# Kernel tuning notes

Hardware: AMD Instinct MI355X
Metric: run time of the kernel (lower is better)

Reference implementation:

```python
import jax, jax.numpy as jnp
import numpy as np

B, T, N, K, DEG = 4, 256, 4096, 64, 4
L = T - 1                # number of transition steps
NNZ = B * N * DEG        # COO entries per step


def setup_inputs() -> dict:
    key = jax.random.key(0)
    k1, k2, k3, k4, k5 = jax.random.split(key, 5)
    observation = jax.random.normal(k1, (B, T, K), dtype=jnp.float32)
    W_em = jax.random.normal(k2, (K, N), dtype=jnp.float32) * 0.05
    duration = jax.random.randint(k3, (B,), 1, T + 1)  # in [1, T]
    # COO layout: for each batch b and each source state s, DEG outgoing edges
    src = jnp.tile(jnp.repeat(jnp.arange(N, dtype=jnp.int32), DEG), (B,))   # [NNZ]
    bidx = jnp.repeat(jnp.arange(B, dtype=jnp.int32), N * DEG)              # [NNZ]
    tgt = jax.random.randint(k4, (L, NNZ), 0, N, dtype=jnp.int32)
    # guarantee a self-loop so every target state has >=1 incoming edge
    self_mask = (jnp.arange(NNZ) % DEG) == 0
    tgt = jnp.where(self_mask[None, :], src[None, :], tgt)
    trans_idx = jnp.stack([jnp.broadcast_to(bidx, (L, NNZ)),
                           jnp.broadcast_to(src, (L, NNZ)),
                           tgt], axis=-1)                                   # [L,NNZ,3]
    trans_logvals = jnp.log(jax.random.uniform(k5, (L, NNZ), minval=0.1, maxval=1.0,
                                               dtype=jnp.float32))
    return {"observation": observation, "W_em": W_em, "duration": duration,
            "trans_idx": trans_idx, "trans_logvals": trans_logvals}


def _forward_alpha(observation, W_em, trans_idx, trans_logvals):
    # emission log-probs [B,T,N]
    em = jax.nn.log_softmax(jnp.einsum('btk,kn->btn', observation, W_em), axis=-1)
    la0 = em[:, 0, :] - jnp.log(jnp.float32(N))  # uniform start distribution

    def step(la_prev, inp):
        idx, lv, e = inp  # idx [NNZ,3], lv [NNZ], e [B,N]
        b, s, t = idx[:, 0], idx[:, 1], idx[:, 2]
        seg = b * N + t
        contrib = la_prev[b, s] + lv  # log_alpha[b,src] + log A[b,src,tgt]
        # numerically-stable segmented logsumexp over incoming edges per (b,tgt)
        m = jax.ops.segment_max(contrib, seg, num_segments=B * N)
        m_safe = jnp.where(jnp.isfinite(m), m, 0.0)
        ssum = jax.ops.segment_sum(jnp.exp(contrib - m_safe[seg]), seg,
                                   num_segments=B * N)
        ssum_safe = jnp.where(ssum > 0, ssum, 1.0)
        la = jnp.where(ssum > 0, jnp.log(ssum_safe) + m_safe, -jnp.inf)
        la = la.reshape(B, N) + e
        return la, la

    em_t = jnp.swapaxes(em, 0, 1)  # [T,B,N]
    _, las = jax.lax.scan(step, la0, (trans_idx, trans_logvals, em_t[1:]))
    log_alpha = jnp.concatenate([la0[None], las], axis=0)  # [T,B,N]
    return jnp.swapaxes(log_alpha, 0, 1)  # [B,T,N]


def reference(observation, W_em, duration, trans_idx, trans_logvals):
    log_alpha = _forward_alpha(observation, W_em, trans_idx, trans_logvals)
    log_sums = jax.nn.logsumexp(log_alpha, axis=2)                # [B,T]
    log_probs = jnp.take_along_axis(log_sums, duration[:, None] - 1, axis=1)  # [B,1]
    return log_probs
```

## Files before the change

### kernel.cpp

```cpp
#include <hip/hip_runtime.h>
#include <hip/hip_bf16.h>

#define Bc 4
#define Tc 256
#define Nc 4096
#define Kc 64
#define DEGc 4
#define Lc (Tc - 1)
#define NNZc (Bc * Nc * DEGc)
#define NPB 8
#define TPB 512
#define TPB_EM 256
#define NODES_PER (Nc / NPB)
#define INV_N (1.0f / 4096.0f)

typedef float f32x4 __attribute__((ext_vector_type(4)));

__device__ __forceinline__ float cohLoadF(const float* p) {
  return __hip_atomic_load((float*)p, __ATOMIC_RELAXED, __HIP_MEMORY_SCOPE_AGENT);
}
__device__ __forceinline__ void cohStore4(float* p, f32x4 v) {
  asm volatile("global_store_dwordx4 %0, %1, off sc0 sc1" :: "v"(p), "v"(v) : "memory");
}

template <int NT>
__device__ __forceinline__ float blockSumT(float v, volatile float* red) {
#pragma unroll
  for (int o = 1; o < 64; o <<= 1) v += __shfl_xor(v, o, 64);
  __syncthreads();
  if ((threadIdx.x & 63) == 0) red[threadIdx.x >> 6] = v;
  __syncthreads();
  float s = 0.f;
#pragma unroll
  for (int k = 0; k < NT / 64; ++k) s += red[k];
  return s;
}
template <int NT>
__device__ __forceinline__ float blockMaxT(float v, volatile float* red) {
#pragma unroll
  for (int o = 1; o < 64; o <<= 1) v = fmaxf(v, __shfl_xor(v, o, 64));
  __syncthreads();
  if ((threadIdx.x & 63) == 0) red[threadIdx.x >> 6] = v;
  __syncthreads();
  float m = -INFINITY;
#pragma unroll
  for (int k = 0; k < NT / 64; ++k) m = fmaxf(m, red[k]);
  return m;
}

__global__ __launch_bounds__(TPB_EM) void em_kernel(const float* __restrict__ obs,
                                                    const float* __restrict__ W,
                                                    float* __restrict__ emexp) {
  const int r = blockIdx.x, tid = threadIdx.x;
  __shared__ float o[Kc];
  __shared__ float red[8];
  if (tid < Kc) o[tid] = obs[(size_t)r * Kc + tid];
  __syncthreads();
  float4 acc[4];
#pragma unroll
  for (int gI = 0; gI < 4; ++gI) acc[gI] = make_float4(0.f, 0.f, 0.f, 0.f);
  const float4* W4 = (const float4*)W;
  for (int k = 0; k < Kc; ++k) {
    const float ov = o[k];
    const float4* wr = W4 + (size_t)k * (Nc / 4);
#pragma unroll
    for (int gI = 0; gI < 4; ++gI) {
      float4 w = wr[gI * 256 + tid];
      acc[gI].x = fmaf(ov, w.x, acc[gI].x);
      acc[gI].y = fmaf(ov, w.y, acc[gI].y);
      acc[gI].z = fmaf(ov, w.z, acc[gI].z);
      acc[gI].w = fmaf(ov, w.w, acc[gI].w);
    }
  }
  float m = -INFINITY;
#pragma unroll
  for (int gI = 0; gI < 4; ++gI)
    m = fmaxf(m, fmaxf(fmaxf(acc[gI].x, acc[gI].y), fmaxf(acc[gI].z, acc[gI].w)));
  m = blockMaxT<TPB_EM>(m, red);
  float s = 0.f;
#pragma unroll
  for (int gI = 0; gI < 4; ++gI)
    s += __expf(acc[gI].x - m) + __expf(acc[gI].y - m) + __expf(acc[gI].z - m) + __expf(acc[gI].w - m);
  s = blockSumT<TPB_EM>(s, red);
  const float lse = m + __logf(s);
  float4* em4 = (float4*)emexp;
#pragma unroll
  for (int gI = 0; gI < 4; ++gI) {
    float4 w = acc[gI];
    w.x = __expf(w.x - lse); w.y = __expf(w.y - lse);
    w.z = __expf(w.z - lse); w.w = __expf(w.w - lse);
    em4[(size_t)r * (Nc / 4) + gI * 256 + tid] = w;
  }
}

__device__ __forceinline__ void publish(unsigned long long* slot, unsigned t, float sp) {
  union { float f; unsigned u; } c; c.f = sp;
  unsigned long long v = ((unsigned long long)c.u << 32) | (unsigned long long)t;
  __hip_atomic_store(slot, v, __ATOMIC_RELAXED, __HIP_MEMORY_SCOPE_AGENT);
}
__device__ __forceinline__ float pollFlags(unsigned long long* fb, int parity, unsigned t) {
  unsigned long long* base = fb + parity * 8;
  for (;;) {
    unsigned long long v[8];
#pragma unroll
    for (int k = 0; k < 8; ++k)
      v[k] = __hip_atomic_load(&base[k], __ATOMIC_RELAXED, __HIP_MEMORY_SCOPE_AGENT);
    bool ok = true;
    float s = 0.f;
#pragma unroll
    for (int k = 0; k < 8; ++k) {
      ok &= ((unsigned)(v[k] & 0xffffffffull) >= t);
      union { unsigned u; float f; } c; c.u = (unsigned)(v[k] >> 32);
      s += c.f;
    }
    if (ok) return s;
  }
}

__global__ __launch_bounds__(TPB) void scan_kernel(
    const int* __restrict__ duration,
    const int* __restrict__ tidx,
    const float* __restrict__ tlv,
    const float* __restrict__ emexp,
    float* __restrict__ part,
    unsigned long long* __restrict__ flags,
    float* __restrict__ out) {
  const int g = blockIdx.x;
  const int b = g / NPB, sl = g % NPB;
  const int tid = threadIdx.x;
  __shared__ float red[TPB / 64];
  __shared__ float lsb[Nc];
  __shared__ float sprev_sh;

  const int node = sl * NODES_PER + tid;
  const size_t ebase = (size_t)b * (Nc * DEGc) + (size_t)node * DEGc;
  unsigned long long* fb = flags + (size_t)b * 16;
  const int tstar = duration[b] - 1;

#pragma unroll
  for (int i = 0; i < Nc / TPB; ++i) lsb[i * TPB + tid] = 0.f;

  float v = emexp[((size_t)b * Tc) * Nc + node] * INV_N;
  float Spart = blockSumT<TPB>(v, red);
  float inv_sprev = 1.0f;
  float acc = 0.f;

  int4 c0, c1, c2; float4 cl; float em_cur;
  {
    const int4* ip = (const int4*)tidx + ((ebase * 3) >> 2);
    c0 = ip[0]; c1 = ip[1]; c2 = ip[2];
    cl = ((const float4*)tlv)[ebase >> 2];
    em_cur = emexp[((size_t)b * Tc + 1) * Nc + node];
  }

  for (int t = 1; t <= tstar; ++t) {
    const float a = v * inv_sprev;
    atomicAdd(&lsb[c0.z], a * __expf(cl.x));
    atomicAdd(&lsb[c1.y], a * __expf(cl.y));
    atomicAdd(&lsb[c2.x], a * __expf(cl.z));
    atomicAdd(&lsb[c2.w], a * __expf(cl.w));
    __syncthreads();

    float* pp = part + (((size_t)(t & 1) * Bc + b) * NPB + sl) * Nc;
    {
      f32x4 w0 = *(const f32x4*)&lsb[tid * 8];
      f32x4 w1 = *(const f32x4*)&lsb[tid * 8 + 4];
      *(f32x4*)&lsb[tid * 8] = (f32x4)0.0f;
      *(f32x4*)&lsb[tid * 8 + 4] = (f32x4)0.0f;
      cohStore4(&pp[tid * 8], w0);
      cohStore4(&pp[tid * 8 + 4], w1);
    }
    __syncthreads();

    if (tid == 0) {
      asm volatile("s_waitcnt vmcnt(0)" ::: "memory");
      publish(&fb[(t & 1) * 8 + sl], (unsigned)t, Spart);
    }

    int4 m0 = c0, m1 = c1, m2 = c2; float4 ml = cl; float em_nxt = em_cur;
    if (t < tstar) {
      const size_t e = (size_t)t * NNZc + ebase;
      const int4* ip = (const int4*)tidx + ((e * 3) >> 2);
      m0 = ip[0]; m1 = ip[1]; m2 = ip[2];
      ml = ((const float4*)tlv)[e >> 2];
      em_nxt = emexp[((size_t)b * Tc + t + 1) * Nc + node];
    }

    if (tid == 0) {
      float sp = pollFlags(fb, t & 1, (unsigned)t);
      sprev_sh = sp;
      if (sl == 0 && t <= tstar - 1) acc += __logf(sp);
    }
    __syncthreads();
    const float sprev = sprev_sh;

    const float* pbase = part + ((size_t)(t & 1) * Bc + b) * NPB * Nc;
    float pk[NPB];
#pragma unroll
    for (int k = 0; k < NPB; ++k) pk[k] = cohLoadF(&pbase[(size_t)k * Nc + node]);
    float sv = 0.f;
#pragma unroll
    for (int k = 0; k < NPB; ++k) sv += pk[k];
    v = sv * em_cur;
    Spart = blockSumT<TPB>(v, red);
    inv_sprev = __frcp_rn(sprev);

    c0 = m0; c1 = m1; c2 = m2; cl = ml; em_cur = em_nxt;
  }

  __syncthreads();
  if (tid == 0) {
    publish(&fb[((tstar + 1) & 1) * 8 + sl], (unsigned)(tstar + 1), Spart);
    if (sl == 0) {
      float sf = pollFlags(fb, (tstar + 1) & 1, (unsigned)(tstar + 1));
      out[b] = acc + __logf(sf);
    }
  }
}

extern "C" void kernel_launch(void* const* d_in, const int* in_sizes, int n_in,
                              void* d_out, int out_size, void* d_ws, size_t ws_size,
                              hipStream_t stream) {
  const float* obs = (const float*)d_in[0];
  const float* W = (const float*)d_in[1];
  const int* duration = (const int*)d_in[2];
  const int* tidx = (const int*)d_in[3];
  const float* tlv = (const float*)d_in[4];
  float* out = (float*)d_out;

  float* emexp = (float*)d_ws;
  float* part = emexp + (size_t)Bc * Tc * Nc;
  unsigned long long* flags = (unsigned long long*)(part + (size_t)2 * Bc * NPB * Nc);

  (void)hipMemsetAsync(flags, 0, Bc * 16 * sizeof(unsigned long long), stream);

  em_kernel<<<dim3(Bc * Tc), dim3(TPB_EM), 0, stream>>>(obs, W, emexp);
  scan_kernel<<<dim3(Bc * NPB), dim3(TPB), 0, stream>>>(duration, tidx, tlv, emexp,
                                                        part, flags, out);
}
```

Measured before the change: 1.775 ms.

## Pre-sort transitions by target into CSR and run single-block-per-batch pull scan

Adds a parallel sort kernel that buckets every step's COO edges by target state into a packed CSR (16-bit source plus fp16 edge weight) with row offsets. The sequential scan then runs as one 1024-thread block per batch that gathers incoming edges from shared memory. This replaces the shared-memory atomic scatter and the cross-block flag polling used before. The emission kernel now computes four timesteps per block and skips timesteps beyond each batch's duration. The trade-offs are fp16 rounding of transition probabilities and less parallelism in the serial scan, with only four blocks active.

```diff
diff --git a/kernel.cpp b/kernel.cpp
--- a/kernel.cpp
+++ b/kernel.cpp
@@ -1,27 +1,19 @@
 #include <hip/hip_runtime.h>
-#include <hip/hip_bf16.h>
+#include <hip/hip_fp16.h>
+
 
 #define Bc 4
 #define Tc 256
 #define Nc 4096
 #define Kc 64
-#define DEGc 4
 #define Lc (Tc - 1)
-#define NNZc (Bc * Nc * DEGc)
-#define NPB 8
-#define TPB 512
-#define TPB_EM 256
-#define NODES_PER (Nc / NPB)
+#define NNZb (Nc * 4)
+#define NNZc (Bc * NNZb)
+#define EROW 4104
 #define INV_N (1.0f / 4096.0f)
 
-typedef float f32x4 __attribute__((ext_vector_type(4)));
-
-__device__ __forceinline__ float cohLoadF(const float* p) {
-  return __hip_atomic_load((float*)p, __ATOMIC_RELAXED, __HIP_MEMORY_SCOPE_AGENT);
-}
-__device__ __forceinline__ void cohStore4(float* p, f32x4 v) {
-  asm volatile("global_store_dwordx4 %0, %1, off sc0 sc1" :: "v"(p), "v"(v) : "memory");
-}
+typedef unsigned int u32;
+typedef unsigned short u16;
 
 template <int NT>
 __device__ __forceinline__ float blockSumT(float v, volatile float* red) {
@@ -48,174 +40,233 @@
   return m;
 }
 
-__global__ __launch_bounds__(TPB_EM) void em_kernel(const float* __restrict__ obs,
-                                                    const float* __restrict__ W,
-                                                    float* __restrict__ emexp) {
-  const int r = blockIdx.x, tid = threadIdx.x;
-  __shared__ float o[Kc];
+__global__ __launch_bounds__(256) void em_kernel(const float* __restrict__ obs,
+                                                 const float* __restrict__ W,
+                                                 const int* __restrict__ duration,
+                                                 float* __restrict__ emexp) {
+  const int blk = blockIdx.x, tid = threadIdx.x;
+  const int b = blk >> 6;
+  const int t0 = (blk & 63) << 2;
+  if (t0 > duration[b] - 1) return;
+  const int rbase = b * Tc + t0;
+  __shared__ float osh[4][Kc];
   __shared__ float red[8];
-  if (tid < Kc) o[tid] = obs[(size_t)r * Kc + tid];
-  __syncthreads();
-  float4 acc[4];
-#pragma unroll
-  for (int gI = 0; gI < 4; ++gI) acc[gI] = make_float4(0.f, 0.f, 0.f, 0.f);
+  osh[tid >> 6][tid & 63] = obs[(size_t)(rbase + (tid >> 6)) * Kc + (tid & 63)];
+  __syncthreads();
+  float4 acc[4][4];
+#pragma unroll
+  for (int r = 0; r < 4; ++r)
+#pragma unroll
+    for (int g = 0; g < 4; ++g) acc[r][g] = make_float4(0.f, 0.f, 0.f, 0.f);
   const float4* W4 = (const float4*)W;
   for (int k = 0; k < Kc; ++k) {
-    const float ov = o[k];
-    const float4* wr = W4 + (size_t)k * (Nc / 4);
-#pragma unroll
-    for (int gI = 0; gI < 4; ++gI) {
-      float4 w = wr[gI * 256 + tid];
-      acc[gI].x = fmaf(ov, w.x, acc[gI].x);
-      acc[gI].y = fmaf(ov, w.y, acc[gI].y);
-      acc[gI].z = fmaf(ov, w.z, acc[gI].z);
-      acc[gI].w = fmaf(ov, w.w, acc[gI].w);
-    }
-  }
-  float m = -INFINITY;
-#pragma unroll
-  for (int gI = 0; gI < 4; ++gI)
-    m = fmaxf(m, fmaxf(fmaxf(acc[gI].x, acc[gI].y), fmaxf(acc[gI].z, acc[gI].w)));
-  m = blockMaxT<TPB_EM>(m, red);
+#pragma unroll
+    for (int g = 0; g < 4; ++g) {
+      const float4 w = W4[(size_t)k * (Nc / 4) + g * 256 + tid];
+#pragma unroll
+      for (int r = 0; r < 4; ++r) {
+        const float ov = osh[r][k];
+        acc[r][g].x = fmaf(ov, w.x, acc[r][g].x);
+        acc[r][g].y = fmaf(ov, w.y, acc[r][g].y);
+        acc[r][g].z = fmaf(ov, w.z, acc[r][g].z);
+        acc[r][g].w = fmaf(ov, w.w, acc[r][g].w);
+      }
+    }
+  }
+  float4* em4 = (float4*)emexp;
+#pragma unroll
+  for (int r = 0; r < 4; ++r) {
+    float m = -INFINITY;
+#pragma unroll
+    for (int g = 0; g < 4; ++g)
+      m = fmaxf(m, fmaxf(fmaxf(acc[r][g].x, acc[r][g].y), fmaxf(acc[r][g].z, acc[r][g].w)));
+    m = blockMaxT<256>(m, red);
+    float s = 0.f;
+#pragma unroll
+    for (int g = 0; g < 4; ++g)
+      s += __expf(acc[r][g].x - m) + __expf(acc[r][g].y - m) +
+           __expf(acc[r][g].z - m) + __expf(acc[r][g].w - m);
+    s = blockSumT<256>(s, red);
+    const float lse = m + __logf(s);
+#pragma unroll
+    for (int g = 0; g < 4; ++g) {
+      float4 w = acc[r][g];
+      w.x = __expf(w.x - lse); w.y = __expf(w.y - lse);
+      w.z = __expf(w.z - lse); w.w = __expf(w.w - lse);
+      em4[(size_t)(rbase + r) * (Nc / 4) + g * 256 + tid] = w;
+    }
+  }
+}
+
+__global__ __launch_bounds__(1024) void sort_kernel(const int* __restrict__ duration,
+                                                    const int* __restrict__ tidx,
+                                                    const float* __restrict__ tlv,
+                                                    u32* __restrict__ ce,
+                                                    u16* __restrict__ ends) {
+  const int rb = blockIdx.x;
+  const int b = rb & 3, row = rb >> 2;
+  if (row > duration[b] - 2) return;
+  const int tid = threadIdx.x;
+  __shared__ u32 cnt[Nc];
+  __shared__ u32 wred[16];
+  *(uint4*)&cnt[tid << 2] = make_uint4(0, 0, 0, 0);
+  __syncthreads();
+
+  const size_t ebase = (size_t)row * NNZc + (size_t)b * NNZb + (size_t)(tid << 4);
+  const int4* ip = (const int4*)tidx + ((ebase * 3) >> 2);
+  int4 c[12];
+#pragma unroll
+  for (int i = 0; i < 12; ++i) c[i] = ip[i];
+  const float4* lp = (const float4*)tlv + (ebase >> 2);
+  float4 lv[4];
+#pragma unroll
+  for (int g = 0; g < 4; ++g) lv[g] = lp[g];
+  u32 tg[16];
+#pragma unroll
+  for (int g = 0; g < 4; ++g) {
+    tg[4 * g + 0] = (u32)c[3 * g + 0].z;
+    tg[4 * g + 1] = (u32)c[3 * g + 1].y;
+    tg[4 * g + 2] = (u32)c[3 * g + 2].x;
+    tg[4 * g + 3] = (u32)c[3 * g + 2].w;
+  }
+#pragma unroll
+  for (int k = 0; k < 16; ++k) atomicAdd(&cnt[tg[k]], 1u);
+  __syncthreads();
+
+  uint4 c4 = *(uint4*)&cnt[tid << 2];
+  const u32 s = c4.x + c4.y + c4.z + c4.w;
+  u32 sc = s;
+#pragma unroll
+  for (int o = 1; o < 64; o <<= 1) {
+    u32 nv = __shfl_up(sc, o, 64);
+    if ((tid & 63) >= o) sc += nv;
+  }
+  if ((tid & 63) == 63) wred[tid >> 6] = sc;
+  __syncthreads();
+  if (tid < 64) {
+    u32 wv = (tid < 16) ? wred[tid] : 0;
+#pragma unroll
+    for (int o = 1; o < 16; o <<= 1) {
+      u32 nv = __shfl_up(wv, o, 64);
+      if (tid >= o) wv += nv;
+    }
+    if (tid < 16) wred[tid] = wv;
+  }
+  __syncthreads();
+  const u32 base = sc - s + ((tid >> 6) ? wred[(tid >> 6) - 1] : 0u);
+  cnt[(tid << 2) + 0] = base;
+  cnt[(tid << 2) + 1] = base + c4.x;
+  cnt[(tid << 2) + 2] = base + c4.x + c4.y;
+  cnt[(tid << 2) + 3] = base + c4.x + c4.y + c4.z;
+  __syncthreads();
+
+  u32* ceRow = ce + (size_t)rb * NNZb;
+#pragma unroll
+  for (int g = 0; g < 4; ++g) {
+    const u32 src = (u32)((tid << 2) + g);
+    const float l0 = lv[g].x, l1 = lv[g].y, l2 = lv[g].z, l3 = lv[g].w;
+    u32 pos;
+    pos = atomicAdd(&cnt[tg[4 * g + 0]], 1u);
+    ceRow[pos] = src | ((u32)__half_as_ushort(__float2half_rn(__expf(l0))) << 16);
+    pos = atomicAdd(&cnt[tg[4 * g + 1]], 1u);
+    ceRow[pos] = src | ((u32)__half_as_ushort(__float2half_rn(__expf(l1))) << 16);
+    pos = atomicAdd(&cnt[tg[4 * g + 2]], 1u);
+    ceRow[pos] = src | ((u32)__half_as_ushort(__float2half_rn(__expf(l2))) << 16);
+    pos = atomicAdd(&cnt[tg[4 * g + 3]], 1u);
+    ceRow[pos] = src | ((u32)__half_as_ushort(__float2half_rn(__expf(l3))) << 16);
+  }
+  __syncthreads();
+
+  u16* eRow = ends + (size_t)rb * EROW;
+  if (tid == 0) eRow[0] = 0;
+#pragma unroll
+  for (int i = 0; i < 4; ++i) eRow[1 + (tid << 2) + i] = (u16)cnt[(tid << 2) + i];
+}
+
+__device__ __forceinline__ float bsum1024(float x, volatile float* red) {
+#pragma unroll
+  for (int o = 1; o < 64; o <<= 1) x += __shfl_xor(x, o, 64);
+  if ((threadIdx.x & 63) == 0) red[threadIdx.x >> 6] = x;
+  __syncthreads();
   float s = 0.f;
 #pragma unroll
-  for (int gI = 0; gI < 4; ++gI)
-    s += __expf(acc[gI].x - m) + __expf(acc[gI].y - m) + __expf(acc[gI].z - m) + __expf(acc[gI].w - m);
-  s = blockSumT<TPB_EM>(s, red);
-  const float lse = m + __logf(s);
-  float4* em4 = (float4*)emexp;
-#pragma unroll
-  for (int gI = 0; gI < 4; ++gI) {
-    float4 w = acc[gI];
-    w.x = __expf(w.x - lse); w.y = __expf(w.y - lse);
-    w.z = __expf(w.z - lse); w.w = __expf(w.w - lse);
-    em4[(size_t)r * (Nc / 4) + gI * 256 + tid] = w;
-  }
-}
-
-__device__ __forceinline__ void publish(unsigned long long* slot, unsigned t, float sp) {
-  union { float f; unsigned u; } c; c.f = sp;
-  unsigned long long v = ((unsigned long long)c.u << 32) | (unsigned long long)t;
-  __hip_atomic_store(slot, v, __ATOMIC_RELAXED, __HIP_MEMORY_SCOPE_AGENT);
-}
-__device__ __forceinline__ float pollFlags(unsigned long long* fb, int parity, unsigned t) {
-  unsigned long long* base = fb + parity * 8;
-  for (;;) {
-    unsigned long long v[8];
-#pragma unroll
-    for (int k = 0; k < 8; ++k)
-      v[k] = __hip_atomic_load(&base[k], __ATOMIC_RELAXED, __HIP_MEMORY_SCOPE_AGENT);
-    bool ok = true;
-    float s = 0.f;
-#pragma unroll
-    for (int k = 0; k < 8; ++k) {
-      ok &= ((unsigned)(v[k] & 0xffffffffull) >= t);
-      union { unsigned u; float f; } c; c.u = (unsigned)(v[k] >> 32);
-      s += c.f;
-    }
-    if (ok) return s;
-  }
-}
-
-__global__ __launch_bounds__(TPB) void scan_kernel(
-    const int* __restrict__ duration,
-    const int* __restrict__ tidx,
-    const float* __restrict__ tlv,
-    const float* __restrict__ emexp,
-    float* __restrict__ part,
-    unsigned long long* __restrict__ flags,
-    float* __restrict__ out) {
-  const int g = blockIdx.x;
-  const int b = g / NPB, sl = g % NPB;
-  const int tid = threadIdx.x;
-  __shared__ float red[TPB / 64];
-  __shared__ float lsb[Nc];
-  __shared__ float sprev_sh;
-
-  const int node = sl * NODES_PER + tid;
-  const size_t ebase = (size_t)b * (Nc * DEGc) + (size_t)node * DEGc;
-  unsigned long long* fb = flags + (size_t)b * 16;
+  for (int k = 0; k < 16; ++k) s += red[k];
+  return s;
+}
+
+__global__ __launch_bounds__(1024) void scan_kernel(const int* __restrict__ duration,
+                                                    const u32* __restrict__ ce,
+                                                    const u16* __restrict__ ends,
+                                                    const float* __restrict__ emexp,
+                                                    float* __restrict__ out) {
+  const int b = blockIdx.x, tid = threadIdx.x;
+  __shared__ float A[Nc];
+  __shared__ float red[16];
   const int tstar = duration[b] - 1;
-
-#pragma unroll
-  for (int i = 0; i < Nc / TPB; ++i) lsb[i * TPB + tid] = 0.f;
-
-  float v = emexp[((size_t)b * Tc) * Nc + node] * INV_N;
-  float Spart = blockSumT<TPB>(v, red);
-  float inv_sprev = 1.0f;
-  float acc = 0.f;
-
-  int4 c0, c1, c2; float4 cl; float em_cur;
-  {
-    const int4* ip = (const int4*)tidx + ((ebase * 3) >> 2);
-    c0 = ip[0]; c1 = ip[1]; c2 = ip[2];
-    cl = ((const float4*)tlv)[ebase >> 2];
-    em_cur = emexp[((size_t)b * Tc + 1) * Nc + node];
-  }
+  const float4* em4 = (const float4*)emexp;
+  const size_t embase = (size_t)b * Tc;
+
+  const float4 em0 = em4[embase * (Nc / 4) + tid];
+  float4 v = make_float4(em0.x * INV_N, em0.y * INV_N, em0.z * INV_N, em0.w * INV_N);
+  float S = bsum1024(v.x + v.y + v.z + v.w, red);
+  float logacc = __logf(S);
+  float iv = __frcp_rn(S);
+  *(float4*)&A[tid << 2] = make_float4(v.x * iv, v.y * iv, v.z * iv, v.w * iv);
+
+  uint2 pe = make_uint2(0, 0);
+  u32 pe4 = 0;
+  float4 pem = make_float4(0.f, 0.f, 0.f, 0.f);
+  if (tstar >= 1) {
+    const u16* er = ends + (size_t)b * EROW;
+    pe = *(const uint2*)(er + (tid << 2));
+    pe4 = er[(tid << 2) + 4];
+    pem = em4[(embase + 1) * (Nc / 4) + tid];
+  }
+  __syncthreads();
 
   for (int t = 1; t <= tstar; ++t) {
-    const float a = v * inv_sprev;
-    atomicAdd(&lsb[c0.z], a * __expf(cl.x));
-    atomicAdd(&lsb[c1.y], a * __expf(cl.y));
-    atomicAdd(&lsb[c2.x], a * __expf(cl.z));
-    atomicAdd(&lsb[c2.w], a * __expf(cl.w));
+    const u32 b0 = pe.x & 0xFFFFu, b1 = pe.x >> 16;
+    const u32 b2 = pe.y & 0xFFFFu, b3 = pe.y >> 16, b4 = pe4;
+    const u32* ceRow = ce + (size_t)(((t - 1) << 2) + b) * NNZb;
+    const float4 emt = pem;
+
+    if (t < tstar) {
+      const u16* er = ends + (size_t)((t << 2) + b) * EROW;
+      pe = *(const uint2*)(er + (tid << 2));
+      pe4 = er[(tid << 2) + 4];
+      pem = em4[(embase + t + 1) * (Nc / 4) + tid];
+    }
+
+    float y0 = 0.f, y1 = 0.f, y2 = 0.f, y3 = 0.f;
+    const u32 n = b4 - b0;
+    u32 p0 = ceRow[b0], p1 = ceRow[b0 + 1], p2 = ceRow[b0 + 2], p3 = ceRow[b0 + 3];
+    for (u32 j = 0; j < n; j += 4) {
+      const u32 q0 = p0, q1 = p1, q2 = p2, q3 = p3;
+      const u32 nj = b0 + j + 4;
+      p0 = ceRow[nj]; p1 = ceRow[nj + 1]; p2 = ceRow[nj + 2]; p3 = ceRow[nj + 3];
+#define PROC(Q, K)                                                                    \
+      {                                                                               \
+        const u32 idx = b0 + j + (K);                                                 \
+        float f = __half2float(__ushort_as_half((u16)((Q) >> 16))) * A[(Q) & 0xFFFFu];\
+        f = (idx < b4) ? f : 0.f;                                                     \
+        y0 += (idx < b1) ? f : 0.f;                                                   \
+        y1 += (idx >= b1 && idx < b2) ? f : 0.f;                                      \
+        y2 += (idx >= b2 && idx < b3) ? f : 0.f;                                      \
+        y3 += (idx >= b3) ? f : 0.f;                                                  \
+      }
+      PROC(q0, 0) PROC(q1, 1) PROC(q2, 2) PROC(q3, 3)
+#undef PROC
+    }
+
+    v.x = y0 * emt.x; v.y = y1 * emt.y; v.z = y2 * emt.z; v.w = y3 * emt.w;
+    const float S_ = bsum1024(v.x + v.y + v.z + v.w, red);
+    logacc += __logf(S_);
+    const float iv_ = __frcp_rn(S_);
+    *(float4*)&A[tid << 2] = make_float4(v.x * iv_, v.y * iv_, v.z * iv_, v.w * iv_);
     __syncthreads();
-
-    float* pp = part + (((size_t)(t & 1) * Bc + b) * NPB + sl) * Nc;
-    {
-      f32x4 w0 = *(const f32x4*)&lsb[tid * 8];
-      f32x4 w1 = *(const f32x4*)&lsb[tid * 8 + 4];
-      *(f32x4*)&lsb[tid * 8] = (f32x4)0.0f;
-      *(f32x4*)&lsb[tid * 8 + 4] = (f32x4)0.0f;
-      cohStore4(&pp[tid * 8], w0);
-      cohStore4(&pp[tid * 8 + 4], w1);
-    }
-    __syncthreads();
-
-    if (tid == 0) {
-      asm volatile("s_waitcnt vmcnt(0)" ::: "memory");
-      publish(&fb[(t & 1) * 8 + sl], (unsigned)t, Spart);
-    }
-
-    int4 m0 = c0, m1 = c1, m2 = c2; float4 ml = cl; float em_nxt = em_cur;
-    if (t < tstar) {
-      const size_t e = (size_t)t * NNZc + ebase;
-      const int4* ip = (const int4*)tidx + ((e * 3) >> 2);
-      m0 = ip[0]; m1 = ip[1]; m2 = ip[2];
-      ml = ((const float4*)tlv)[e >> 2];
-      em_nxt = emexp[((size_t)b * Tc + t + 1) * Nc + node];
-    }
-
-    if (tid == 0) {
-      float sp = pollFlags(fb, t & 1, (unsigned)t);
-      sprev_sh = sp;
-      if (sl == 0 && t <= tstar - 1) acc += __logf(sp);
-    }
-    __syncthreads();
-    const float sprev = sprev_sh;
-
-    const float* pbase = part + ((size_t)(t & 1) * Bc + b) * NPB * Nc;
-    float pk[NPB];
-#pragma unroll
-    for (int k = 0; k < NPB; ++k) pk[k] = cohLoadF(&pbase[(size_t)k * Nc + node]);
-    float sv = 0.f;
-#pragma unroll
-    for (int k = 0; k < NPB; ++k) sv += pk[k];
-    v = sv * em_cur;
-    Spart = blockSumT<TPB>(v, red);
-    inv_sprev = __frcp_rn(sprev);
-
-    c0 = m0; c1 = m1; c2 = m2; cl = ml; em_cur = em_nxt;
-  }
-
-  __syncthreads();
-  if (tid == 0) {
-    publish(&fb[((tstar + 1) & 1) * 8 + sl], (unsigned)(tstar + 1), Spart);
-    if (sl == 0) {
-      float sf = pollFlags(fb, (tstar + 1) & 1, (unsigned)(tstar + 1));
-      out[b] = acc + __logf(sf);
-    }
-  }
+  }
+
+  if (tid == 0) out[b] = logacc;
 }
 
 extern "C" void kernel_launch(void* const* d_in, const int* in_sizes, int n_in,
@@ -229,12 +280,10 @@
   float* out = (float*)d_out;
 
   float* emexp = (float*)d_ws;
-  float* part = emexp + (size_t)Bc * Tc * Nc;
-  unsigned long long* flags = (unsigned long long*)(part + (size_t)2 * Bc * NPB * Nc);
-
-  (void)hipMemsetAsync(flags, 0, Bc * 16 * sizeof(unsigned long long), stream);
-
-  em_kernel<<<dim3(Bc * Tc), dim3(TPB_EM), 0, stream>>>(obs, W, emexp);
-  scan_kernel<<<dim3(Bc * NPB), dim3(TPB), 0, stream>>>(duration, tidx, tlv, emexp,
-                                                        part, flags, out);
-}
+  u32* ce = (u32*)(emexp + (size_t)Bc * Tc * Nc);
+  u16* ends = (u16*)(ce + (size_t)Lc * Bc * NNZb + 32);
+
+  em_kernel<<<dim3(Bc * (Tc / 4)), dim3(256), 0, stream>>>(obs, W, duration, emexp);
+  sort_kernel<<<dim3(Lc * Bc), dim3(1024), 0, stream>>>(duration, tidx, tlv, ce, ends);
+  scan_kernel<<<dim3(Bc), dim3(1024), 0, stream>>>(duration, ce, ends, emexp, out);
+}
```

Result: slower. 2.020 ms (+13.8%).
